# Kernel tuning notes

Hardware: AMD Instinct MI355X
Metric: run time of the kernel (lower is better)

## Reference

```python
import jax, jax.numpy as jnp
import numpy as np

H, D = 8, 64
LN_EPS = 1e-5

def elu_p1(x):
    return jax.nn.elu(x) + 1.0

def sum_norm(x):
    return x / jnp.sum(x, axis=-1, keepdims=True)

def setup_inputs() -> dict:
    key = jax.random.key(0)
    k1, k2, k3 = jax.random.split(key, 3)
    slen, bsz, in_dim = 1024, 32, 512
    x = jax.random.normal(k1, (slen, bsz, in_dim), dtype=jnp.float32)
    ln_gamma = jnp.ones((in_dim,), dtype=jnp.float32)
    ln_beta = jnp.zeros((in_dim,), dtype=jnp.float32)
    # Linear weights stored as [in, out] (transposed vs torch) and fan-in scaled
    w_slow = jax.random.normal(k2, (in_dim, H * (3 * D + 1)), dtype=jnp.float32) / np.sqrt(in_dim)
    w_out = jax.random.normal(k3, (H * D, in_dim), dtype=jnp.float32) / np.sqrt(H * D)
    return {"x": x, "ln_gamma": ln_gamma, "ln_beta": ln_beta, "w_slow": w_slow, "w_out": w_out}

def reference(x, ln_gamma, ln_beta, w_slow, w_out):
    slen, bsz, in_dim = x.shape
    # LayerNorm
    mu = jnp.mean(x, axis=-1, keepdims=True)
    var = jnp.mean((x - mu) ** 2, axis=-1, keepdims=True)
    h = (x - mu) * jax.lax.rsqrt(var + LN_EPS) * ln_gamma + ln_beta
    # slow net projection -> q, k, v, beta per head
    qkvb = (h @ w_slow).reshape(slen, bsz, H, 3 * D + 1)
    q, k, v, beta = jnp.split(qkvb, [D, 2 * D, 3 * D], axis=-1)
    beta = jax.nn.sigmoid(beta)            # [slen, bsz, H, 1]
    q = sum_norm(elu_p1(q))                # [slen, bsz, H, D]
    k = sum_norm(elu_p1(k))
    # delta-rule fast-weight recurrence over time
    W0 = jnp.zeros((bsz, H, D, D), dtype=x.dtype)
    def step(W, inp):
        q_t, k_t, v_t, b_t = inp           # [bsz,H,D], [bsz,H,D], [bsz,H,D], [bsz,H,1]
        v_old = jnp.einsum('bhij,bhj->bhi', W, k_t)
        upd = b_t * (v_t - v_old)          # [bsz,H,D]
        W = W + upd[..., :, None] * k_t[..., None, :]
        o_t = jnp.einsum('bhij,bhj->bhi', W, q_t)
        return W, o_t
    _, outs = jax.lax.scan(step, W0, (q, k, v, beta))  # outs [slen, bsz, H, D]
    out = outs.reshape(slen, bsz, H * D) @ w_out       # [slen, bsz, in_dim]
    return x + out
```

## Files before the change

kernel.cpp:

```cpp
#include <hip/hip_runtime.h>
#include <cstdint>

using short8  = __attribute__((ext_vector_type(8))) short;
using ushort8 = __attribute__((ext_vector_type(8))) unsigned short;
using short4v = __attribute__((ext_vector_type(4))) short;
using f32x4   = __attribute__((ext_vector_type(4))) float;

#define H_    8
#define SLEN  1024
#define BSZ   32
#define INDIM 512
#define NQKV  1544
#define NPAD  1664
#define MROWS 32768
#define PB    72

#define GLOAD16(gp, lp) __builtin_amdgcn_global_load_lds( \
    (const __attribute__((address_space(1))) void*)(gp),  \
    (__attribute__((address_space(3))) void*)(lp), 16, 0, 0)

static __device__ __forceinline__ float bf2f(unsigned short s) {
    return __uint_as_float(((unsigned int)s) << 16);
}
#if defined(__BF16_MANT_DIG__)
static __device__ __forceinline__ unsigned short f2bf(float f) {
    union { __bf16 b; unsigned short u; } cv;
    cv.b = (__bf16)f;
    return cv.u;
}
#else
static __device__ __forceinline__ unsigned short f2bf(float f) {
    unsigned int u = __float_as_uint(f);
    u += 0x7FFFu + ((u >> 16) & 1u);
    return (unsigned short)(u >> 16);
}
#endif

__global__ __launch_bounds__(256) void ln_kernel(const float* __restrict__ x,
                                                 const float* __restrict__ gamma,
                                                 const float* __restrict__ betap,
                                                 unsigned short* __restrict__ h) {
    int row = blockIdx.x * 4 + (threadIdx.x >> 6);
    int l   = threadIdx.x & 63;
    const f32x4* xr = (const f32x4*)(x + (size_t)row * INDIM);
    f32x4 a = xr[l * 2], b = xr[l * 2 + 1];
    float s = 0.f, sq = 0.f;
    #pragma unroll
    for (int j = 0; j < 4; ++j) { s += a[j]; sq += a[j] * a[j]; }
    #pragma unroll
    for (int j = 0; j < 4; ++j) { s += b[j]; sq += b[j] * b[j]; }
    #pragma unroll
    for (int off = 32; off; off >>= 1) { s += __shfl_xor(s, off); sq += __shfl_xor(sq, off); }
    float mean = s * (1.f / 512.f);
    float var  = sq * (1.f / 512.f) - mean * mean;
    float rstd = rsqrtf(var + 1e-5f);
    const f32x4* g4 = (const f32x4*)gamma;
    const f32x4* b4 = (const f32x4*)betap;
    f32x4 g0 = g4[l * 2], g1 = g4[l * 2 + 1], e0 = b4[l * 2], e1 = b4[l * 2 + 1];
    short8 o;
    #pragma unroll
    for (int j = 0; j < 4; ++j) o[j]     = (short)f2bf((a[j] - mean) * rstd * g0[j] + e0[j]);
    #pragma unroll
    for (int j = 0; j < 4; ++j) o[4 + j] = (short)f2bf((b[j] - mean) * rstd * g1[j] + e1[j]);
    ((short8*)(h + (size_t)row * INDIM))[l] = o;
}

__global__ __launch_bounds__(256) void cvt_wslow(const float* __restrict__ w,
                                                 unsigned short* __restrict__ wT) {
    int idx = blockIdx.x * 256 + threadIdx.x;
    int n = idx >> 9, k = idx & 511;
    int c;
    if (n < 512)       c = (n >> 6) * 193 + (n & 63);
    else if (n < 1024) c = ((n - 512) >> 6) * 193 + 64 + (n & 63);
    else if (n < 1536) c = ((n - 1024) >> 6) * 193 + 128 + (n & 63);
    else if (n < 1544) c = (n - 1536) * 193 + 192;
    else               c = -1;
    wT[idx] = (c >= 0) ? f2bf(w[(size_t)k * NQKV + c]) : (unsigned short)0;
}
__global__ __launch_bounds__(256) void cvt_wout(const float* __restrict__ w,
                                                unsigned short* __restrict__ wT) {
    int idx = blockIdx.x * 256 + threadIdx.x;
    int n = idx >> 9, k = idx & 511;
    wT[idx] = f2bf(w[(size_t)k * 512 + n]);
}

__global__ __launch_bounds__(256) void gemm_qkv(const unsigned short* __restrict__ A,
                                                const unsigned short* __restrict__ BT,
                                                unsigned short* __restrict__ qn,
                                                unsigned short* __restrict__ kn,
                                                unsigned short* __restrict__ vn,
                                                float* __restrict__ bet) {
    __shared__ unsigned short As[128 * 64];
    __shared__ unsigned short Bs[128 * 64];
    const int t  = threadIdx.x;
    const int id = blockIdx.y * 13 + blockIdx.x;
    const int newid = (id & 7) * 416 + (id >> 3);
    const int bx = newid % 13;
    const int n0 = bx * 128;
    const int m0 = (newid / 13) * 128;
    const int w = t >> 6, l = t & 63;
    const int wr = (w >> 1) * 64, wc = (w & 1) * 64;
    f32x4 acc[4][4] = {};
    for (int kt = 0; kt < INDIM; kt += 64) {
        __syncthreads();
        #pragma unroll
        for (int c = 0; c < 4; ++c) {
            int idx = c * 256 + t;
            int row = idx >> 3, kc2 = (idx & 7) * 8;
            int lb = (c * 256 + (t & 192)) * 8;
            GLOAD16(A  + (size_t)(m0 + row) * INDIM + kt + kc2, &As[lb]);
            GLOAD16(BT + (size_t)(n0 + row) * INDIM + kt + kc2, &Bs[lb]);
        }
        __syncthreads();
        #pragma unroll
        for (int kk = 0; kk < 2; ++kk) {
            const int kr = kk * 32 + (l >> 4) * 8;
            short8 af[4], bf[4];
            #pragma unroll
            for (int m = 0; m < 4; ++m) af[m] = *(const short8*)&As[(wr + m * 16 + (l & 15)) * 64 + kr];
            #pragma unroll
            for (int n = 0; n < 4; ++n) bf[n] = *(const short8*)&Bs[(wc + n * 16 + (l & 15)) * 64 + kr];
            #pragma unroll
            for (int m = 0; m < 4; ++m)
                #pragma unroll
                for (int n = 0; n < 4; ++n)
                    acc[m][n] = __builtin_amdgcn_mfma_f32_16x16x32_bf16(af[m], bf[n], acc[m][n], 0, 0, 0);
        }
    }
    const int g = l >> 4, cc = l & 15;
    const int colbase = n0 + wc;
    if (bx < 12) {
        const int reg  = colbase >> 9;
        const int head = (colbase >> 6) & 7;
        unsigned short* dst = (reg == 0) ? qn : (reg == 1) ? kn : vn;
        #pragma unroll
        for (int m = 0; m < 4; ++m) {
            #pragma unroll
            for (int j = 0; j < 4; ++j) {
                int row = m0 + wr + m * 16 + g * 4 + j;
                int s = row >> 5, b = row & 31;
                size_t base = ((size_t)(b * H_ + head) * SLEN + s) * 64;
                float e0 = acc[m][0][j], e1 = acc[m][1][j], e2 = acc[m][2][j], e3 = acc[m][3][j];
                if (reg < 2) {
                    e0 = e0 > 0.f ? e0 + 1.f : __expf(e0);
                    e1 = e1 > 0.f ? e1 + 1.f : __expf(e1);
                    e2 = e2 > 0.f ? e2 + 1.f : __expf(e2);
                    e3 = e3 > 0.f ? e3 + 1.f : __expf(e3);
                    float ssum = (e0 + e1) + (e2 + e3);
                    ssum += __shfl_xor(ssum, 1);
                    ssum += __shfl_xor(ssum, 2);
                    ssum += __shfl_xor(ssum, 4);
                    ssum += __shfl_xor(ssum, 8);
                    float inv = 1.f / ssum;
                    e0 *= inv; e1 *= inv; e2 *= inv; e3 *= inv;
                }
                dst[base +  0 + cc] = f2bf(e0);
                dst[base + 16 + cc] = f2bf(e1);
                dst[base + 32 + cc] = f2bf(e2);
                dst[base + 48 + cc] = f2bf(e3);
            }
        }
    } else {
        if (wc == 0 && cc < 8) {
            #pragma unroll
            for (int m = 0; m < 4; ++m)
                #pragma unroll
                for (int j = 0; j < 4; ++j) {
                    int row = m0 + wr + m * 16 + g * 4 + j;
                    int s = row >> 5, b = row & 31;
                    float v = acc[m][0][j];
                    bet[(size_t)(b * H_ + cc) * SLEN + s] = 1.f / (1.f + __expf(-v));
                }
        }
    }
}

__global__ __launch_bounds__(256) void gemm_out(const unsigned short* __restrict__ A,
                                                const unsigned short* __restrict__ BT,
                                                const float* __restrict__ X,
                                                float* __restrict__ outf) {
    __shared__ unsigned short As[128 * 64];
    __shared__ unsigned short Bs[128 * 64];
    const int t  = threadIdx.x;
    const int id = blockIdx.y * 4 + blockIdx.x;
    const int newid = (id & 7) * 128 + (id >> 3);
    const int n0 = (newid % 4) * 128;
    const int m0 = (newid / 4) * 128;
    const int w = t >> 6, l = t & 63;
    const int wr = (w >> 1) * 64, wc = (w & 1) * 64;
    f32x4 acc[4][4] = {};
    for (int kt = 0; kt < INDIM; kt += 64) {
        __syncthreads();
        #pragma unroll
        for (int c = 0; c < 4; ++c) {
            int idx = c * 256 + t;
            int row = idx >> 3, kc2 = (idx & 7) * 8;
            int lb = (c * 256 + (t & 192)) * 8;
            GLOAD16(A  + (size_t)(m0 + row) * INDIM + kt + kc2, &As[lb]);
            GLOAD16(BT + (size_t)(n0 + row) * INDIM + kt + kc2, &Bs[lb]);
        }
        __syncthreads();
        #pragma unroll
        for (int kk = 0; kk < 2; ++kk) {
            const int kr = kk * 32 + (l >> 4) * 8;
            short8 af[4], bf[4];
            #pragma unroll
            for (int m = 0; m < 4; ++m) af[m] = *(const short8*)&As[(wr + m * 16 + (l & 15)) * 64 + kr];
            #pragma unroll
            for (int n = 0; n < 4; ++n) bf[n] = *(const short8*)&Bs[(wc + n * 16 + (l & 15)) * 64 + kr];
            #pragma unroll
            for (int m = 0; m < 4; ++m)
                #pragma unroll
                for (int n = 0; n < 4; ++n)
                    acc[m][n] = __builtin_amdgcn_mfma_f32_16x16x32_bf16(af[m], bf[n], acc[m][n], 0, 0, 0);
        }
    }
    const int rb = (l >> 4) * 4, cc = l & 15;
    #pragma unroll
    for (int m = 0; m < 4; ++m)
        #pragma unroll
        for (int n = 0; n < 4; ++n)
            #pragma unroll
            for (int j = 0; j < 4; ++j) {
                int row = m0 + wr + m * 16 + rb + j;
                int col = n0 + wc + n * 16 + cc;
                size_t o = (size_t)row * 512 + col;
                outf[o] = X[o] + acc[m][n][j];
            }
}

__global__ __launch_bounds__(512, 4) void fwtiles(const unsigned short* __restrict__ qn,
                                                  const unsigned short* __restrict__ kn,
                                                  const unsigned short* __restrict__ vn,
                                                  const float* __restrict__ beta,
                                                  unsigned short* __restrict__ tiles,
                                                  unsigned short* __restrict__ outs) {
    __shared__ unsigned short Ax[64 * PB], Atr[64 * PB], Pw[64 * PB], Pwtr[64 * PB];
    __shared__ unsigned short Z0[128 * PB], Z1[128 * PB];
    __shared__ float bv[64];
    const int bx = blockIdx.x;
    const int bh = bx >> 4, c = bx & 15;
    const int b = bh >> 3, h = bh & 7;
    const int c0 = c * 64;
    const int tid = threadIdx.x;
    const int w = tid >> 6, l = tid & 63;
    const int mw = w & 3, nh = w >> 2;
    const int lr = l & 15, lk = (l >> 4) << 3, rb = (l >> 4) << 2;
    const unsigned short* kc = kn + ((size_t)bh * SLEN + c0) * 64;
    const unsigned short* qc = qn + ((size_t)bh * SLEN + c0) * 64;
    const unsigned short* vc = vn + ((size_t)bh * SLEN + c0) * 64;
    const float* bb = beta + (size_t)bh * SLEN + c0;

    {
        #pragma unroll
        for (int i = 0; i < 2; ++i) {
            int idx = i * 512 + tid;
            int row = idx >> 3, seg = idx & 7;
            const unsigned short* src = (row < 64) ? (vc + (size_t)row * 64 + seg * 8)
                                                   : (kc + (size_t)(row - 64) * 64 + seg * 8);
            *(ushort8*)&Z1[row * PB + seg * 8] = *(const ushort8*)src;
        }
        if (tid < 64) bv[tid] = bb[tid];
        ushort8 z8 = {};
        for (int i = tid; i < 576; i += 512) { ((ushort8*)Ax)[i] = z8; ((ushort8*)Atr)[i] = z8; }
    }
    __syncthreads();

    auto ldb = [&](const unsigned short* M, int m, int kk) -> short8 {
        return *(const short8*)&M[(m * 16 + lr) * PB + kk * 32 + lk];
    };

    {
        const int zoff2 = (w >> 2) * 64;
        const int tbase = (w & 3) * 16;
        const float sgn = (w >= 4) ? -1.f : 1.f;
        ushort8 b0v, b1v;
        #pragma unroll
        for (int i = 0; i < 16; ++i) {
            int r = w * 16 + i;
            float val = sgn * bv[tbase + i] * bf2f(Z1[r * PB + l]);
            unsigned short uv = f2bf(val);
            if (i < 8) b0v[i] = uv; else b1v[i - 8] = uv;
        }
        *(ushort8*)&Z0[(zoff2 + l) * PB + tbase]     = b0v;
        *(ushort8*)&Z0[(zoff2 + l) * PB + tbase + 8] = b1v;
    }
    {
        const int pm[10] = {0, 1, 1, 2, 2, 2, 3, 3, 3, 3};
        const int pn[10] = {0, 0, 1, 0, 1, 2, 0, 1, 2, 3};
        for (int pi = w; pi < 10; pi += 8) {
            int m = pm[pi], n = pn[pi];
            short8 ka0 = *(const short8*)&Z1[(64 + 16 * m + lr) * PB + lk];
            short8 ka1 = *(const short8*)&Z1[(64 + 16 * m + lr) * PB + 32 + lk];
            short8 kb0 = *(const short8*)&Z1[(64 + 16 * n + lr) * PB + lk];
            short8 kb1 = *(const short8*)&Z1[(64 + 16 * n + lr) * PB + 32 + lk];
            f32x4 a = {};
            a = __builtin_amdgcn_mfma_f32_16x16x32_bf16(ka0, kb0, a, 0, 0, 0);
            a = __builtin_amdgcn_mfma_f32_16x16x32_bf16(ka1, kb1, a, 0, 0, 0);
            f32x4 btm = *(const f32x4*)&bv[16 * m + rb];
            short4v pk;
            #pragma unroll
            for (int j = 0; j < 4; ++j) {
                int tt = 16 * m + rb + j, s = 16 * n + lr;
                unsigned short v = (s < tt) ? f2bf(-btm[j] * a[j]) : (unsigned short)0;
                Ax[tt * PB + s] = v;
                pk[j] = (short)v;
            }
            *(short4v*)&Atr[(16 * n + lr) * PB + 16 * m + rb] = pk;
        }
    }
    __syncthreads();

    auto zprod = [&](const unsigned short* Xb, int p, const unsigned short* Zs, unsigned short* Zd) {
        const bool msk0 = (16 * mw + 15 >= p), msk1 = (16 * mw + 15 - 32 >= p);
        short8 xf0, xf1;
        if (msk0) xf0 = ldb(Xb, mw, 0);
        if (msk1) xf1 = ldb(Xb, mw, 1);
        #pragma unroll
        for (int ni = 0; ni < 4; ++ni) {
            int n = nh * 4 + ni;
            short4v zi = *(const short4v*)&Zs[(16 * n + lr) * PB + 16 * mw + rb];
            f32x4 a;
            #pragma unroll
            for (int j = 0; j < 4; ++j) a[j] = bf2f((unsigned short)zi[j]);
            if (msk0) a = __builtin_amdgcn_mfma_f32_16x16x32_bf16(xf0, ldb(Zs, n, 0), a, 0, 0, 0);
            if (msk1) a = __builtin_amdgcn_mfma_f32_16x16x32_bf16(xf1, ldb(Zs, n, 1), a, 0, 0, 0);
            short4v zo;
            #pragma unroll
            for (int j = 0; j < 4; ++j) zo[j] = (short)f2bf(a[j]);
            *(short4v*)&Zd[(16 * n + lr) * PB + 16 * mw + rb] = zo;
        }
    };
    auto powp = [&](const unsigned short* Ps, const unsigned short* Pstr, int p,
                    unsigned short* Pd, unsigned short* Pdtr) {
        const bool x0 = (16 * mw + 15 >= p), x1 = (16 * mw + 15 - 32 >= p);
        short8 xf0, xf1;
        if (x0) xf0 = ldb(Ps, mw, 0);
        if (x1) xf1 = ldb(Ps, mw, 1);
        #pragma unroll
        for (int ni = 0; ni < 2; ++ni) {
            int n = nh * 2 + ni;
            const bool y0 = (31 - 16 * n >= p), y1 = (63 - 16 * n >= p);
            f32x4 a = {};
            if (x0 && y0) a = __builtin_amdgcn_mfma_f32_16x16x32_bf16(xf0, ldb(Pstr, n, 0), a, 0, 0, 0);
            if (x1 && y1) a = __builtin_amdgcn_mfma_f32_16x16x32_bf16(xf1, ldb(Pstr, n, 1), a, 0, 0, 0);
            short4v pk;
            #pragma unroll
            for (int j = 0; j < 4; ++j) {
                unsigned short v = f2bf(a[j]);
                Pd[(16 * mw + rb + j) * PB + 16 * n + lr] = v;
                pk[j] = (short)v;
            }
            *(short4v*)&Pdtr[(16 * n + lr) * PB + 16 * mw + rb] = pk;
        }
    };

    zprod(Ax, 1, Z0, Z1);  powp(Ax, Atr, 1, Pw, Pwtr);  __syncthreads();
    zprod(Pw, 2, Z1, Z0);  powp(Pw, Pwtr, 2, Ax, Atr);  __syncthreads();
    zprod(Ax, 4, Z0, Z1);  powp(Ax, Atr, 4, Pw, Pwtr);  __syncthreads();
    zprod(Pw, 8, Z1, Z0);  powp(Pw, Pwtr, 8, Ax, Atr);  __syncthreads();
    zprod(Ax, 16, Z0, Z1); powp(Ax, Atr, 16, Pw, Pwtr); __syncthreads();
    zprod(Pw, 32, Z1, Z0);
    __syncthreads();

    {
        #pragma unroll
        for (int i = 0; i < 2; ++i) {
            int idx = i * 512 + tid;
            int row = idx >> 3, seg = idx & 7;
            const unsigned short* src = (row < 64) ? (qc + (size_t)row * 64 + seg * 8)
                                                   : (kc + (size_t)(row - 64) * 64 + seg * 8);
            *(ushort8*)&Z1[row * PB + seg * 8] = *(const ushort8*)src;
        }
    }
    __syncthreads();

    {
        short8 qa0 = *(const short8*)&Z1[(16 * mw + lr) * PB + lk];
        short8 qa1 = *(const short8*)&Z1[(16 * mw + lr) * PB + 32 + lk];
        #pragma unroll
        for (int ni = 0; ni < 2; ++ni) {
            int n = nh * 2 + ni;
            short8 kb0 = *(const short8*)&Z1[(64 + 16 * n + lr) * PB + lk];
            short8 kb1 = *(const short8*)&Z1[(64 + 16 * n + lr) * PB + 32 + lk];
            f32x4 a = {};
            a = __builtin_amdgcn_mfma_f32_16x16x32_bf16(qa0, kb0, a, 0, 0, 0);
            a = __builtin_amdgcn_mfma_f32_16x16x32_bf16(qa1, kb1, a, 0, 0, 0);
            #pragma unroll
            for (int j = 0; j < 4; ++j) {
                int tt = 16 * mw + rb + j, s = 16 * n + lr;
                Ax[tt * PB + s] = (s <= tt) ? f2bf(a[j]) : (unsigned short)0;
            }
        }
        ushort8 kv;
        #pragma unroll
        for (int j = 0; j < 8; ++j)
            kv[j] = Z1[(64 + w * 8 + j) * PB + l];
        *(ushort8*)&Pwtr[l * PB + w * 8] = kv;
    }
    __syncthreads();

    {
        unsigned short* tb = tiles + ((size_t)bh * 16 + c) * 12288;
        short8 pA0 = ldb(Ax, mw, 0), pA1 = ldb(Ax, mw, 1);
        short8 zA0 = ldb(Z0, mw, 0), zA1 = ldb(Z0, mw, 1);
        short8 kt0 = ldb(Pwtr, mw, 0), kt1 = ldb(Pwtr, mw, 1);
        #pragma unroll
        for (int ni = 0; ni < 2; ++ni) {
            int n = nh * 2 + ni;
            f32x4 aN = {};
            aN = __builtin_amdgcn_mfma_f32_16x16x32_bf16(zA0, ldb(Pwtr, n, 0), aN, 0, 0, 0);
            aN = __builtin_amdgcn_mfma_f32_16x16x32_bf16(zA1, ldb(Pwtr, n, 1), aN, 0, 0, 0);
            f32x4 aM = {};
            aM = __builtin_amdgcn_mfma_f32_16x16x32_bf16(kt0, ldb(Z0, 4 + n, 0), aM, 0, 0, 0);
            aM = __builtin_amdgcn_mfma_f32_16x16x32_bf16(kt1, ldb(Z0, 4 + n, 1), aM, 0, 0, 0);
            f32x4 aG;
            #pragma unroll
            for (int j = 0; j < 4; ++j) aG[j] = bf2f(Z1[(16 * mw + rb + j) * PB + 16 * n + lr]);
            aG = __builtin_amdgcn_mfma_f32_16x16x32_bf16(pA0, ldb(Z0, 4 + n, 0), aG, 0, 0, 0);
            aG = __builtin_amdgcn_mfma_f32_16x16x32_bf16(pA1, ldb(Z0, 4 + n, 1), aG, 0, 0, 0);
            f32x4 aP = {};
            aP = __builtin_amdgcn_mfma_f32_16x16x32_bf16(pA0, ldb(Z0, n, 0), aP, 0, 0, 0);
            aP = __builtin_amdgcn_mfma_f32_16x16x32_bf16(pA1, ldb(Z0, n, 1), aP, 0, 0, 0);
            #pragma unroll
            for (int j = 0; j < 4; ++j) {
                int r = 16 * mw + rb + j, cl = 16 * n + lr;
                tb[r * 64 + cl]        = f2bf(aM[j]);
                tb[4096 + r * 64 + cl] = f2bf(aG[j]);
                tb[8192 + r * 64 + cl] = f2bf(aN[j]);
                outs[((size_t)(c0 + r) * BSZ + b) * 512 + h * 64 + cl] = f2bf(aP[j]);
            }
        }
    }
}

__global__ __launch_bounds__(256) void fwscan_w(const unsigned short* __restrict__ tiles,
                                                unsigned short* __restrict__ wchk) {
    __shared__ float Wf[64 * 68];
    const int bh = blockIdx.x;
    const int tid = threadIdx.x;
    const int w = tid >> 6, l = tid & 63;
    const int lr = l & 15, lk = (l >> 4) << 3, rb = (l >> 4) << 2;
    const int cr = l >> 3, cc8 = (l & 7) * 8;
    #pragma unroll
    for (int j = 0; j < 16; ++j) Wf[(16 * w + j) * 68 + l] = 0.f;

    const unsigned short* tb0 = tiles + (size_t)bh * 16 * 12288;
    unsigned short* wc0 = wchk + (size_t)bh * 16 * 4096;

    auto loadc = [&](short8 (&MT)[4][2], unsigned short (&NV)[4][4], int c) {
        const unsigned short* tb = tb0 + (size_t)c * 12288;
        #pragma unroll
        for (int n = 0; n < 4; ++n) {
            MT[n][0] = *(const short8*)(tb + (size_t)(16 * n + lr) * 64 + lk);
            MT[n][1] = *(const short8*)(tb + (size_t)(16 * n + lr) * 64 + 32 + lk);
            #pragma unroll
            for (int j = 0; j < 4; ++j)
                NV[n][j] = tb[8192 + (size_t)(16 * w + rb + j) * 64 + 16 * n + lr];
        }
    };
    auto stepc = [&](short8 (&MT)[4][2], unsigned short (&NV)[4][4], int c) {
        #pragma unroll
        for (int half = 0; half < 2; ++half) {
            int row = 16 * w + half * 8 + cr;
            const float* p = &Wf[row * 68 + cc8];
            f32x4 x0 = *(const f32x4*)p, x1 = *(const f32x4*)(p + 4);
            ushort8 o;
            #pragma unroll
            for (int j = 0; j < 4; ++j) { o[j] = f2bf(x0[j]); o[4 + j] = f2bf(x1[j]); }
            *(ushort8*)(wc0 + (size_t)c * 4096 + row * 64 + cc8) = o;
        }
        short8 wf0, wf1;
        {
            const float* p0 = &Wf[(16 * w + lr) * 68 + lk];
            f32x4 a0 = *(const f32x4*)p0, b0 = *(const f32x4*)(p0 + 4);
            f32x4 a1 = *(const f32x4*)(p0 + 32), b1 = *(const f32x4*)(p0 + 36);
            #pragma unroll
            for (int j = 0; j < 4; ++j) {
                wf0[j] = (short)f2bf(a0[j]); wf0[4 + j] = (short)f2bf(b0[j]);
                wf1[j] = (short)f2bf(a1[j]); wf1[4 + j] = (short)f2bf(b1[j]);
            }
        }
        #pragma unroll
        for (int n = 0; n < 4; ++n) {
            f32x4 a;
            #pragma unroll
            for (int j = 0; j < 4; ++j)
                a[j] = Wf[(16 * w + rb + j) * 68 + 16 * n + lr] + bf2f(NV[n][j]);
            a = __builtin_amdgcn_mfma_f32_16x16x32_bf16(wf0, MT[n][0], a, 0, 0, 0);
            a = __builtin_amdgcn_mfma_f32_16x16x32_bf16(wf1, MT[n][1], a, 0, 0, 0);
            #pragma unroll
            for (int j = 0; j < 4; ++j) Wf[(16 * w + rb + j) * 68 + 16 * n + lr] = a[j];
        }
    };

    short8 mtA[4][2], mtB[4][2];
    unsigned short nvA[4][4], nvB[4][4];
    loadc(mtA, nvA, 0);
    #pragma unroll 1
    for (int cc = 0; cc < 8; ++cc) {
        int c = 2 * cc;
        if (c + 1 < 16) loadc(mtB, nvB, c + 1);
        stepc(mtA, nvA, c);
        if (c + 2 < 16) loadc(mtA, nvA, c + 2);
        stepc(mtB, nvB, c + 1);
    }
}

__global__ __launch_bounds__(256) void fw_o(const unsigned short* __restrict__ tiles,
                                            const unsigned short* __restrict__ wchk,
                                            unsigned short* __restrict__ outs) {
    __shared__ unsigned short Ot[64 * 72];
    const int c = blockIdx.x + 1;
    const int bh = blockIdx.y;
    const int b = bh >> 3, h = bh & 7;
    const int c0 = c * 64;
    const int tid = threadIdx.x;
    const int w = tid >> 6, l = tid & 63;
    const int lr = l & 15, lk = (l >> 4) << 3, rb = (l >> 4) << 2;
    const unsigned short* G  = tiles + ((size_t)bh * 16 + c) * 12288 + 4096;
    const unsigned short* W0 = wchk + ((size_t)bh * 16 + c) * 4096;

    #pragma unroll
    for (int i = 0; i < 2; ++i) {
        int idx = i * 256 + tid;
        int t = idx >> 3, d0 = (idx & 7) * 8;
        *(ushort8*)&Ot[t * 72 + d0] =
            *(const ushort8*)(outs + ((size_t)(c0 + t) * BSZ + b) * 512 + h * 64 + d0);
    }
    __syncthreads();

    short8 g0 = *(const short8*)(G + (size_t)(16 * w + lr) * 64 + lk);
    short8 g1 = *(const short8*)(G + (size_t)(16 * w + lr) * 64 + 32 + lk);
    #pragma unroll
    for (int n = 0; n < 4; ++n) {
        short8 wf0 = *(const short8*)(W0 + (size_t)(16 * n + lr) * 64 + lk);
        short8 wf1 = *(const short8*)(W0 + (size_t)(16 * n + lr) * 64 + 32 + lk);
        f32x4 a;
        #pragma unroll
        for (int j = 0; j < 4; ++j) a[j] = bf2f(Ot[(16 * w + rb + j) * 72 + 16 * n + lr]);
        a = __builtin_amdgcn_mfma_f32_16x16x32_bf16(g0, wf0, a, 0, 0, 0);
        a = __builtin_amdgcn_mfma_f32_16x16x32_bf16(g1, wf1, a, 0, 0, 0);
        #pragma unroll
        for (int j = 0; j < 4; ++j) Ot[(16 * w + rb + j) * 72 + 16 * n + lr] = f2bf(a[j]);
    }
    __syncthreads();

    #pragma unroll
    for (int i = 0; i < 2; ++i) {
        int idx = i * 256 + tid;
        int t = idx >> 3, d0 = (idx & 7) * 8;
        *(ushort8*)(outs + ((size_t)(c0 + t) * BSZ + b) * 512 + h * 64 + d0) =
            *(const ushort8*)&Ot[t * 72 + d0];
    }
}

extern "C" void kernel_launch(void* const* d_in, const int* in_sizes, int n_in,
                              void* d_out, int out_size, void* d_ws, size_t ws_size,
                              hipStream_t stream) {
    const float* x      = (const float*)d_in[0];
    const float* g      = (const float*)d_in[1];
    const float* be     = (const float*)d_in[2];
    const float* w_slow = (const float*)d_in[3];
    const float* w_out  = (const float*)d_in[4];
    float* out = (float*)d_out;
    char* ws = (char*)d_ws;

    unsigned short* h    = (unsigned short*)(ws);
    unsigned short* outs = (unsigned short*)(ws);
    unsigned short* qn   = (unsigned short*)(ws + 33554432);
    unsigned short* wchk = (unsigned short*)(ws + 33554432);
    unsigned short* kn   = (unsigned short*)(ws + 67108864);
    unsigned short* vn   = (unsigned short*)(ws + 100663296);
    float*          bet  = (float*)         (ws + 134217728);
    unsigned short* wsT  = (unsigned short*)(ws + 135266304);
    unsigned short* woT  = (unsigned short*)(ws + 136970240);
    unsigned short* tiles= (unsigned short*)(ws + 137494528);

    if (ws_size < 238157824) return;

    ln_kernel<<<8192, 256, 0, stream>>>(x, g, be, h);
    cvt_wslow<<<(NPAD * 512) / 256, 256, 0, stream>>>(w_slow, wsT);
    cvt_wout<<<(512 * 512) / 256, 256, 0, stream>>>(w_out, woT);
    gemm_qkv<<<dim3(13, MROWS / 128), 256, 0, stream>>>(h, wsT, qn, kn, vn, bet);
    fwtiles<<<BSZ * H_ * 16, 512, 0, stream>>>(qn, kn, vn, bet, tiles, outs);
    fwscan_w<<<BSZ * H_, 256, 0, stream>>>(tiles, wchk);
    fw_o<<<dim3(15, BSZ * H_), 256, 0, stream>>>(tiles, wchk, outs);
    gemm_out<<<dim3(4, MROWS / 128), 256, 0, stream>>>(outs, woT, x, out);
}
```

Measured before the change: 344.7 us.

## Enlarge QKV GEMM tiles to 256x256 with double-buffered async LDS loads

Rewrites the QKV projection GEMM to use 256x256 output tiles with 512 threads and double-buffered LDS. Global-to-LDS loads for the next K slice are issued while MFMAs run on the current buffer, with explicit vmcnt waits and barriers. The padded weight width grows to 1792 columns so the N dimension tiles evenly, and the workspace offsets shift to fit. The aim is more reuse per loaded tile and hidden load latency, in exchange for more LDS (128KB per block), higher register pressure from 32 accumulators per lane, and wasted work on the extra padded columns.

```diff
diff --git a/kernel.cpp b/kernel.cpp
--- a/kernel.cpp
+++ b/kernel.cpp
@@ -11,13 +11,21 @@
 #define BSZ   32
 #define INDIM 512
 #define NQKV  1544
-#define NPAD  1664
+#define NPAD2 1792
 #define MROWS 32768
 #define PB    72
 
 #define GLOAD16(gp, lp) __builtin_amdgcn_global_load_lds( \
     (const __attribute__((address_space(1))) void*)(gp),  \
     (__attribute__((address_space(3))) void*)(lp), 16, 0, 0)
+
+#define VMCNT8() do { asm volatile("s_waitcnt vmcnt(8)" ::: "memory"); \
+                      __builtin_amdgcn_sched_barrier(0); } while (0)
+#define VMCNT0() do { asm volatile("s_waitcnt vmcnt(0)" ::: "memory"); \
+                      __builtin_amdgcn_sched_barrier(0); } while (0)
+#define SBAR()   do { __builtin_amdgcn_sched_barrier(0); \
+                      __builtin_amdgcn_s_barrier(); \
+                      __builtin_amdgcn_sched_barrier(0); } while (0)
 
 static __device__ __forceinline__ float bf2f(unsigned short s) {
     return __uint_as_float(((unsigned int)s) << 16);
@@ -84,63 +92,95 @@
     wT[idx] = f2bf(w[(size_t)k * 512 + n]);
 }
 
-__global__ __launch_bounds__(256) void gemm_qkv(const unsigned short* __restrict__ A,
-                                                const unsigned short* __restrict__ BT,
-                                                unsigned short* __restrict__ qn,
-                                                unsigned short* __restrict__ kn,
-                                                unsigned short* __restrict__ vn,
-                                                float* __restrict__ bet) {
-    __shared__ unsigned short As[128 * 64];
-    __shared__ unsigned short Bs[128 * 64];
-    const int t  = threadIdx.x;
-    const int id = blockIdx.y * 13 + blockIdx.x;
-    const int newid = (id & 7) * 416 + (id >> 3);
-    const int bx = newid % 13;
-    const int n0 = bx * 128;
-    const int m0 = (newid / 13) * 128;
-    const int w = t >> 6, l = t & 63;
-    const int wr = (w >> 1) * 64, wc = (w & 1) * 64;
-    f32x4 acc[4][4] = {};
-    for (int kt = 0; kt < INDIM; kt += 64) {
-        __syncthreads();
-        #pragma unroll
-        for (int c = 0; c < 4; ++c) {
-            int idx = c * 256 + t;
+__global__ __launch_bounds__(512, 2) void gemm_qkv(const unsigned short* __restrict__ A,
+                                                   const unsigned short* __restrict__ BT,
+                                                   unsigned short* __restrict__ qn,
+                                                   unsigned short* __restrict__ kn,
+                                                   unsigned short* __restrict__ vn,
+                                                   float* __restrict__ bet) {
+    __shared__ unsigned short As[2][256 * 64];
+    __shared__ unsigned short Bs[2][256 * 64];
+    const int tid = threadIdx.x;
+    const int id = blockIdx.y * 7 + blockIdx.x;
+    const int newid = (id & 7) * 112 + (id >> 3);
+    const int bx = newid % 7;
+    const int n0 = bx * 256;
+    const int m0 = (newid / 7) * 256;
+    const int w = tid >> 6, l = tid & 63;
+    const int wm = w >> 2, wn = w & 3;
+    const int lr = l & 15, lk8 = (l >> 4) * 8;
+    f32x4 acc[8][4] = {};
+
+    auto STAGE = [&](int buf, int kt) {
+        #pragma unroll
+        for (int c2 = 0; c2 < 4; ++c2) {
+            int idx = c2 * 512 + tid;
             int row = idx >> 3, kc2 = (idx & 7) * 8;
-            int lb = (c * 256 + (t & 192)) * 8;
-            GLOAD16(A  + (size_t)(m0 + row) * INDIM + kt + kc2, &As[lb]);
-            GLOAD16(BT + (size_t)(n0 + row) * INDIM + kt + kc2, &Bs[lb]);
-        }
-        __syncthreads();
-        #pragma unroll
-        for (int kk = 0; kk < 2; ++kk) {
-            const int kr = kk * 32 + (l >> 4) * 8;
-            short8 af[4], bf[4];
-            #pragma unroll
-            for (int m = 0; m < 4; ++m) af[m] = *(const short8*)&As[(wr + m * 16 + (l & 15)) * 64 + kr];
-            #pragma unroll
-            for (int n = 0; n < 4; ++n) bf[n] = *(const short8*)&Bs[(wc + n * 16 + (l & 15)) * 64 + kr];
-            #pragma unroll
-            for (int m = 0; m < 4; ++m)
+            int lb = (c2 * 512 + (tid & 448)) * 8;
+            GLOAD16(A  + (size_t)(m0 + row) * INDIM + kt + kc2, &As[buf][lb]);
+            GLOAD16(BT + (size_t)(n0 + row) * INDIM + kt + kc2, &Bs[buf][lb]);
+        }
+    };
+    auto COMPUTE = [&](int buf) {
+        short8 bf2[4][2];
+        #pragma unroll
+        for (int ni = 0; ni < 4; ++ni)
+            #pragma unroll
+            for (int kk = 0; kk < 2; ++kk)
+                bf2[ni][kk] = *(const short8*)&Bs[buf][(wn * 64 + ni * 16 + lr) * 64 + kk * 32 + lk8];
+        #pragma unroll
+        for (int p = 0; p < 4; ++p) {
+            short8 af[2][2];
+            #pragma unroll
+            for (int d = 0; d < 2; ++d)
                 #pragma unroll
-                for (int n = 0; n < 4; ++n)
-                    acc[m][n] = __builtin_amdgcn_mfma_f32_16x16x32_bf16(af[m], bf[n], acc[m][n], 0, 0, 0);
-        }
-    }
+                for (int kk = 0; kk < 2; ++kk)
+                    af[d][kk] = *(const short8*)&As[buf][(wm * 128 + (2 * p + d) * 16 + lr) * 64 + kk * 32 + lk8];
+            #pragma unroll
+            for (int d = 0; d < 2; ++d)
+                #pragma unroll
+                for (int ni = 0; ni < 4; ++ni)
+                    #pragma unroll
+                    for (int kk = 0; kk < 2; ++kk)
+                        acc[2 * p + d][ni] =
+                            __builtin_amdgcn_mfma_f32_16x16x32_bf16(af[d][kk], bf2[ni][kk], acc[2 * p + d][ni], 0, 0, 0);
+        }
+    };
+
+    STAGE(0, 0);
+    STAGE(1, 64);
+    #pragma unroll
+    for (int tp = 0; tp < 4; ++tp) {
+        VMCNT8();
+        SBAR();
+        COMPUTE(0);
+        SBAR();
+        if (tp < 3) {
+            STAGE(0, (2 * tp + 2) * 64);
+            VMCNT8();
+        } else {
+            VMCNT0();
+        }
+        SBAR();
+        COMPUTE(1);
+        SBAR();
+        if (tp < 3) STAGE(1, (2 * tp + 3) * 64);
+    }
+
     const int g = l >> 4, cc = l & 15;
-    const int colbase = n0 + wc;
-    if (bx < 12) {
+    const int colbase = n0 + wn * 64;
+    if (bx < 6) {
         const int reg  = colbase >> 9;
         const int head = (colbase >> 6) & 7;
         unsigned short* dst = (reg == 0) ? qn : (reg == 1) ? kn : vn;
         #pragma unroll
-        for (int m = 0; m < 4; ++m) {
+        for (int mi = 0; mi < 8; ++mi) {
             #pragma unroll
             for (int j = 0; j < 4; ++j) {
-                int row = m0 + wr + m * 16 + g * 4 + j;
+                int row = m0 + wm * 128 + mi * 16 + g * 4 + j;
                 int s = row >> 5, b = row & 31;
                 size_t base = ((size_t)(b * H_ + head) * SLEN + s) * 64;
-                float e0 = acc[m][0][j], e1 = acc[m][1][j], e2 = acc[m][2][j], e3 = acc[m][3][j];
+                float e0 = acc[mi][0][j], e1 = acc[mi][1][j], e2 = acc[mi][2][j], e3 = acc[mi][3][j];
                 if (reg < 2) {
                     e0 = e0 > 0.f ? e0 + 1.f : __expf(e0);
                     e1 = e1 > 0.f ? e1 + 1.f : __expf(e1);
@@ -161,14 +201,14 @@
             }
         }
     } else {
-        if (wc == 0 && cc < 8) {
-            #pragma unroll
-            for (int m = 0; m < 4; ++m)
+        if (wn == 0 && cc < 8) {
+            #pragma unroll
+            for (int mi = 0; mi < 8; ++mi)
                 #pragma unroll
                 for (int j = 0; j < 4; ++j) {
-                    int row = m0 + wr + m * 16 + g * 4 + j;
+                    int row = m0 + wm * 128 + mi * 16 + g * 4 + j;
                     int s = row >> 5, b = row & 31;
-                    float v = acc[m][0][j];
+                    float v = acc[mi][0][j];
                     bet[(size_t)(b * H_ + cc) * SLEN + s] = 1.f / (1.f + __expf(-v));
                 }
         }
@@ -574,15 +614,15 @@
     unsigned short* vn   = (unsigned short*)(ws + 100663296);
     float*          bet  = (float*)         (ws + 134217728);
     unsigned short* wsT  = (unsigned short*)(ws + 135266304);
-    unsigned short* woT  = (unsigned short*)(ws + 136970240);
-    unsigned short* tiles= (unsigned short*)(ws + 137494528);
-
-    if (ws_size < 238157824) return;
+    unsigned short* woT  = (unsigned short*)(ws + 137101312);
+    unsigned short* tiles= (unsigned short*)(ws + 137625600);
+
+    if (ws_size < 238288896) return;
 
     ln_kernel<<<8192, 256, 0, stream>>>(x, g, be, h);
-    cvt_wslow<<<(NPAD * 512) / 256, 256, 0, stream>>>(w_slow, wsT);
+    cvt_wslow<<<(NPAD2 * 512) / 256, 256, 0, stream>>>(w_slow, wsT);
     cvt_wout<<<(512 * 512) / 256, 256, 0, stream>>>(w_out, woT);
-    gemm_qkv<<<dim3(13, MROWS / 128), 256, 0, stream>>>(h, wsT, qn, kn, vn, bet);
+    gemm_qkv<<<dim3(7, MROWS / 256), 512, 0, stream>>>(h, wsT, qn, kn, vn, bet);
     fwtiles<<<BSZ * H_ * 16, 512, 0, stream>>>(qn, kn, vn, bet, tiles, outs);
     fwscan_w<<<BSZ * H_, 256, 0, stream>>>(tiles, wchk);
     fw_o<<<dim3(15, BSZ * H_), 256, 0, stream>>>(tiles, wchk, outs);
```

Result: no change. 339.6 us (-1.5%).
